# Performance work log

Hardware: AMD Instinct MI355X
Metric: run time of the kernel (lower is better)

Reference implementation:

```python
import jax, jax.numpy as jnp
import numpy as np

EMBED_DIM = 128
HEADS = 1
HEAD_DIM = EMBED_DIM // HEADS
TOPK = 3


def setup_inputs() -> dict:
    key = jax.random.key(0)
    k1, k2, k3, k4, k5 = jax.random.split(key, 5)
    N, T, C = 8, 2048, EMBED_DIM
    s = 1.0 / np.sqrt(C)
    return {
        "embeddings": jax.random.normal(k1, (N, T, C), dtype=jnp.float32),
        "ac": jax.random.normal(k2, (N,), dtype=jnp.float32),  # unused by forward (as in source)
        "Wq": jax.random.normal(k3, (C, C), dtype=jnp.float32) * s,
        "Wk": jax.random.normal(k4, (C, C), dtype=jnp.float32) * s,
        "Wo": jax.random.normal(k5, (C, C), dtype=jnp.float32) * s,
        "bo": jnp.zeros((C,), dtype=jnp.float32),
    }


def reference(embeddings, ac, Wq, Wk, Wo, bo):
    N, T, C = embeddings.shape
    H, D = HEADS, HEAD_DIM
    # values are the raw embeddings (no projection), per the source
    values = embeddings.reshape(N, T, H, D)
    keys = (embeddings @ Wk.T).reshape(N, T, H, D)
    queries = (embeddings @ Wq.T).reshape(N, T, H, D)
    # [N,H,T,T] dense scores, scaled by sqrt(embed_dim)
    scores = jnp.einsum('nqhd,nkhd->nhqk', queries, keys) / jnp.sqrt(jnp.float32(C))
    # top-3 masking: keep top-3 per row, -inf elsewhere, then softmax
    topv, topi = jax.lax.top_k(scores, TOPK)  # [N,H,T,3]
    ni = jnp.arange(N)[:, None, None, None]
    hi = jnp.arange(H)[None, :, None, None]
    qi = jnp.arange(T)[None, None, :, None]
    masked = jnp.full(scores.shape, -jnp.inf, scores.dtype).at[ni, hi, qi, topi].set(topv)
    attention = jax.nn.softmax(masked, axis=-1)  # [N,H,T,T]
    out = jnp.einsum('nhql,nlhd->nqhd', attention, values).reshape(N, T, H * D)
    out = out @ Wo.T + bo
    return out, attention
```

## Files before the change

### kernel.cpp

```cpp
#include <hip/hip_runtime.h>
#include <stdint.h>

#define TS 2048
#define CD 128
#define NB 8
#define NROWS (NB*TS)
#define RPB 8
#define SCALE 0.08838834764831845f

#define JSPLIT 8
#define QT 64
#define KT 32
#define KRANGE (TS/JSPLIT)
#define NKT (KRANGE/KT)
#define CSTR 97

typedef _Float16 f16x8 __attribute__((ext_vector_type(8)));
typedef float    f32x4 __attribute__((ext_vector_type(4)));

__device__ __forceinline__ void gload_lds16(const void* g, void* l) {
    __builtin_amdgcn_global_load_lds(
        (const __attribute__((address_space(1))) void*)g,
        (__attribute__((address_space(3))) void*)l, 16, 0, 0);
}

__global__ __launch_bounds__(128) void proj_qk(
    const float* __restrict__ E, const float* __restrict__ Wq,
    const float* __restrict__ Wk, _Float16* __restrict__ Qc, _Float16* __restrict__ Kc)
{
    const int r0 = blockIdx.x * RPB, t = threadIdx.x;
    __shared__ float e[RPB][CD];
    {
        const float4* src = (const float4*)(E + (size_t)r0*CD);
        float4* dst = (float4*)&e[0][0];
        dst[t] = src[t];
        dst[t + 128] = src[t + 128];
    }
    __syncthreads();
    const float* wq = Wq + (size_t)t*CD;
    const float* wk = Wk + (size_t)t*CD;
    float aq[RPB], ak[RPB];
    #pragma unroll
    for (int i = 0; i < RPB; i++) { aq[i] = 0.f; ak[i] = 0.f; }
    #pragma unroll
    for (int c = 0; c < CD; c += 4) {
        float4 a = *(const float4*)(wq + c);
        float4 b = *(const float4*)(wk + c);
        #pragma unroll
        for (int i = 0; i < RPB; i++) {
            float e0 = e[i][c+0], e1 = e[i][c+1], e2 = e[i][c+2], e3 = e[i][c+3];
            aq[i] += a.x*e0 + a.y*e1 + a.z*e2 + a.w*e3;
            ak[i] += b.x*e0 + b.y*e1 + b.z*e2 + b.w*e3;
        }
    }
    #pragma unroll
    for (int i = 0; i < RPB; i++) {
        float q = aq[i], k = ak[i];
        _Float16 qh = (_Float16)q, kh = (_Float16)k;
        _Float16 ql = (_Float16)(q - (float)qh);
        _Float16 kl = (_Float16)(k - (float)kh);
        const size_t rb = (size_t)(r0+i)*256;
        Qc[rb + t] = qh; Qc[rb + 128 + t] = ql;
        Kc[rb + t] = kh; Kc[rb + 128 + t] = kl;
    }
}

#define UPD(v, jg, s) do { \
    if ((v) > tv2[s]) { \
        if ((v) > tv0[s]) { tv2[s]=tv1[s]; ti2[s]=ti1[s]; tv1[s]=tv0[s]; ti1[s]=ti0[s]; tv0[s]=(v); ti0[s]=(jg); } \
        else if ((v) > tv1[s]) { tv2[s]=tv1[s]; ti2[s]=ti1[s]; tv1[s]=(v); ti1[s]=(jg); } \
        else { tv2[s]=(v); ti2[s]=(jg); } \
    } \
} while (0)

__global__ __launch_bounds__(256, 4) void scores_top3(
    const _Float16* __restrict__ Qc, const _Float16* __restrict__ Kc,
    float* __restrict__ SPL)
{
    const int bid = blockIdx.x;
    const int swz = (bid & 7) * 256 + (bid >> 3);
    const int n  = swz >> 8;
    const int sp = (swz >> 5) & 7;
    const int qt = swz & 31;
    const int q0 = qt * QT;
    const int j0 = sp * KRANGE;
    const int tid = threadIdx.x;
    const int w = tid >> 6, l = tid & 63;
    const int m = l & 15, hi = l >> 4;

    __shared__ __align__(16) char lds[32768];

    f16x8 qa[2][4];
    {
        const char* qb = (const char*)Qc + (size_t)(n*TS + q0 + w*16)*512;
        #pragma unroll
        for (int h = 0; h < 2; h++)
            #pragma unroll
            for (int c4 = 0; c4 < 4; c4++)
                qa[h][c4] = *(const f16x8*)(qb + m*512 + h*256 + c4*64 + hi*16);
    }

    const char* kcb = (const char*)Kc + (size_t)(n*TS + j0)*512;
    const char* ps[4];
    {
        const int ksub = l >> 5, coff = (l & 31) * 16;
        #pragma unroll
        for (int i = 0; i < 4; i++) {
            const int key = w*8 + i*2 + ksub;
            ps[i] = kcb + key*512 + (coff ^ ((i*2 + ksub) << 4));
        }
    }
    char* ldsw = lds + w*4096;

    float tv0[4], tv1[4], tv2[4];
    int   ti0[4], ti1[4], ti2[4];
    #pragma unroll
    for (int s = 0; s < 4; s++) {
        tv0[s]=tv1[s]=tv2[s] = -3e38f;
        ti0[s]=ti1[s]=ti2[s] = 0x7fffffff;
    }

    #pragma unroll
    for (int i = 0; i < 4; i++)
        gload_lds16(ps[i], ldsw + i*1024);

    const int swzl = (l & 7) << 4;
    const int lo16 = hi << 4;

    int cur = 0;
    #pragma unroll 1
    for (int kt = 0; kt < NKT; kt++) {
        __syncthreads();
        if (kt + 1 < NKT) {
            char* d_ = ldsw + ((cur^1) << 14);
            #pragma unroll
            for (int i = 0; i < 4; i++)
                gload_lds16(ps[i] + (size_t)(kt+1)*16384, d_ + i*1024);
        }
        const char* kb = lds + (cur << 14);

        f32x4 acc[2];
        acc[0] = (f32x4){0.f,0.f,0.f,0.f};
        acc[1] = (f32x4){0.f,0.f,0.f,0.f};

        __builtin_amdgcn_s_setprio(1);
        #pragma unroll
        for (int ct = 0; ct < 2; ct++) {
            const char* bb = kb + (size_t)(ct*16 + m)*512;
            f16x8 kh[4];
            #pragma unroll
            for (int c4 = 0; c4 < 4; c4++)
                kh[c4] = *(const f16x8*)(bb + ((c4*64 + lo16) ^ swzl));
            #pragma unroll
            for (int c4 = 0; c4 < 4; c4++)
                acc[ct] = __builtin_amdgcn_mfma_f32_16x16x32_f16(qa[0][c4], kh[c4], acc[ct], 0,0,0);
            #pragma unroll
            for (int c4 = 0; c4 < 4; c4++)
                acc[ct] = __builtin_amdgcn_mfma_f32_16x16x32_f16(qa[1][c4], kh[c4], acc[ct], 0,0,0);
            #pragma unroll
            for (int c4 = 0; c4 < 4; c4++) {
                f16x8 kl = *(const f16x8*)(bb + ((256 + c4*64 + lo16) ^ swzl));
                acc[ct] = __builtin_amdgcn_mfma_f32_16x16x32_f16(qa[0][c4], kl, acc[ct], 0,0,0);
            }
        }
        __builtin_amdgcn_s_setprio(0);

        const int jb = j0 + kt*KT;
        #pragma unroll
        for (int rg = 0; rg < 4; rg++) {
            float a0 = acc[0][rg], a1 = acc[1][rg];
            float mx = fmaxf(a0, a1);
            if (mx > tv2[rg]) {
                UPD(a0, jb + m, rg);
                UPD(a1, jb + 16 + m, rg);
            }
        }
        cur ^= 1;
    }

    __syncthreads();
    float* cand = (float*)lds;
    #pragma unroll
    for (int rg = 0; rg < 4; rg++) {
        const int row = w*16 + hi*4 + rg;
        float* cc = cand + row*CSTR + m*6;
        cc[0] = tv0[rg]; cc[1] = __int_as_float(ti0[rg]);
        cc[2] = tv1[rg]; cc[3] = __int_as_float(ti1[rg]);
        cc[4] = tv2[rg]; cc[5] = __int_as_float(ti2[rg]);
    }
    __syncthreads();
    if (tid < QT) {
        float b0v = -3e38f, b1v = -3e38f, b2v = -3e38f;
        int   b0i = 0x7fffffff, b1i = 0x7fffffff, b2i = 0x7fffffff;
        const float* mm = cand + (size_t)tid*CSTR;
        for (int t2 = 0; t2 < 16; t2++) {
            #pragma unroll
            for (int k = 0; k < 3; k++) {
                float v = mm[t2*6 + 2*k];
                int  id = __float_as_int(mm[t2*6 + 2*k + 1]);
                bool g2 = (v > b2v) || (v == b2v && id < b2i);
                if (g2) {
                    bool g0 = (v > b0v) || (v == b0v && id < b0i);
                    bool g1 = (v > b1v) || (v == b1v && id < b1i);
                    if (g0)      { b2v=b1v;b2i=b1i; b1v=b0v;b1i=b0i; b0v=v;b0i=id; }
                    else if (g1) { b2v=b1v;b2i=b1i; b1v=v;  b1i=id; }
                    else         { b2v=v;  b2i=id; }
                }
            }
        }
        const int row = n*TS + q0 + tid;
        float* dst = SPL + ((size_t)row*JSPLIT + sp)*8;
        dst[0] = b0v; dst[1] = __int_as_float(b0i);
        dst[2] = b1v; dst[3] = __int_as_float(b1i);
        dst[4] = b2v; dst[5] = __int_as_float(b2i);
    }
}

__global__ __launch_bounds__(256) void merge_splits(
    const float* __restrict__ SPL, float* __restrict__ TOP)
{
    const int row = blockIdx.x*256 + threadIdx.x;
    const float* s = SPL + (size_t)row*JSPLIT*8;
    float b0v = -3e38f, b1v = -3e38f, b2v = -3e38f;
    int   b0i = 0x7fffffff, b1i = 0x7fffffff, b2i = 0x7fffffff;
    #pragma unroll
    for (int sp = 0; sp < JSPLIT; sp++) {
        #pragma unroll
        for (int k = 0; k < 3; k++) {
            float v = s[sp*8 + 2*k];
            int  id = __float_as_int(s[sp*8 + 2*k + 1]);
            bool g2 = (v > b2v) || (v == b2v && id < b2i);
            if (g2) {
                bool g0 = (v > b0v) || (v == b0v && id < b0i);
                bool g1 = (v > b1v) || (v == b1v && id < b1i);
                if (g0)      { b2v=b1v;b2i=b1i; b1v=b0v;b1i=b0i; b0v=v;b0i=id; }
                else if (g1) { b2v=b1v;b2i=b1i; b1v=v;  b1i=id; }
                else         { b2v=v;  b2i=id; }
            }
        }
    }
    float e1 = __expf((b1v - b0v)*SCALE);
    float e2 = __expf((b2v - b0v)*SCALE);
    float rz = 1.0f / (1.0f + e1 + e2);
    float* dst = TOP + (size_t)row*8;
    dst[0] = rz; dst[1] = e1*rz; dst[2] = e2*rz;
    int* di = (int*)dst;
    di[4] = b0i; di[5] = b1i; di[6] = b2i;
}

__global__ __launch_bounds__(256) void attn_write(
    const float* __restrict__ TOP, float* __restrict__ A)
{
    const int r = blockIdx.x, t = threadIdx.x;
    const float* s = TOP + (size_t)r*8;
    const int* si = (const int*)s;
    float p0 = s[0], p1 = s[1], p2 = s[2];
    int i0 = si[4], i1 = si[5], i2 = si[6];
    const int col0 = t*8;
    float vals[8];
    #pragma unroll
    for (int u = 0; u < 8; u++) {
        int col = col0 + u;
        float v = 0.f;
        if (col == i0) v = p0;
        if (col == i1) v = p1;
        if (col == i2) v = p2;
        vals[u] = v;
    }
    float4* dst = (float4*)(A + (size_t)r*TS + col0);
    dst[0] = make_float4(vals[0], vals[1], vals[2], vals[3]);
    dst[1] = make_float4(vals[4], vals[5], vals[6], vals[7]);
}

__global__ __launch_bounds__(128) void out_proj(
    const float* __restrict__ E, const float* __restrict__ Wo,
    const float* __restrict__ bo, const float* __restrict__ TOP,
    float* __restrict__ OUT)
{
    const int r0 = blockIdx.x * RPB, t = threadIdx.x;
    const int n = r0 >> 11;
    __shared__ float o[RPB][CD];
    #pragma unroll
    for (int i = 0; i < RPB; i++) {
        const float* s = TOP + (size_t)(r0+i)*8;
        const int* si = (const int*)s;
        const float* e0 = E + ((size_t)n*TS + si[4])*CD;
        const float* e1 = E + ((size_t)n*TS + si[5])*CD;
        const float* e2 = E + ((size_t)n*TS + si[6])*CD;
        o[i][t] = s[0]*e0[t] + s[1]*e1[t] + s[2]*e2[t];
    }
    __syncthreads();
    const float* wr = Wo + (size_t)t*CD;
    float acc[RPB];
    float bias = bo[t];
    #pragma unroll
    for (int i = 0; i < RPB; i++) acc[i] = bias;
    #pragma unroll
    for (int c = 0; c < CD; c += 4) {
        float4 a = *(const float4*)(wr + c);
        #pragma unroll
        for (int i = 0; i < RPB; i++)
            acc[i] += a.x*o[i][c+0] + a.y*o[i][c+1] + a.z*o[i][c+2] + a.w*o[i][c+3];
    }
    #pragma unroll
    for (int i = 0; i < RPB; i++)
        OUT[(size_t)(r0+i)*CD + t] = acc[i];
}

extern "C" void kernel_launch(void* const* d_in, const int* in_sizes, int n_in,
                              void* d_out, int out_size, void* d_ws, size_t ws_size,
                              hipStream_t stream)
{
    const float* E  = (const float*)d_in[0];
    const float* Wq = (const float*)d_in[2];
    const float* Wk = (const float*)d_in[3];
    const float* Wo = (const float*)d_in[4];
    const float* bo = (const float*)d_in[5];

    _Float16* Qc = (_Float16*)d_ws;
    _Float16* Kc = Qc + (size_t)NROWS*256;
    float* TOP   = (float*)(Kc + (size_t)NROWS*256);

    float* OUT = (float*)d_out;
    float* A   = OUT + (size_t)NROWS*CD;
    float* SPL = A;

    proj_qk     <<<NROWS/RPB, 128, 0, stream>>>(E, Wq, Wk, Qc, Kc);
    scores_top3 <<<NB*(TS/QT)*JSPLIT, 256, 0, stream>>>(Qc, Kc, SPL);
    merge_splits<<<NROWS/256, 256, 0, stream>>>(SPL, TOP);
    attn_write  <<<NROWS,     256, 0, stream>>>(TOP, A);
    out_proj    <<<NROWS/RPB, 128, 0, stream>>>(E, Wo, bo, TOP, OUT);
}
```

Before: 284.5 us.

## Double query tile per block and fuse split merge into attention write

The scores kernel now gives each wave 32 query rows instead of 16, so every K fragment read from LDS feeds twice as many MFMAs, and the K tile is shared across 128 queries per block. That halves K global/LDS traffic per query but raises register pressure, and occupancy is lowered to 3 blocks per CU. When the workspace is large enough, split candidates go to workspace instead of the attention buffer, and the merge plus dense attention write become one kernel. This removes one launch and the TOP round trip at the cost of every thread redundantly merging its row's splits.

```diff
diff --git a/kernel.cpp b/kernel.cpp
--- a/kernel.cpp
+++ b/kernel.cpp
@@ -9,11 +9,12 @@
 #define SCALE 0.08838834764831845f
 
 #define JSPLIT 8
-#define QT 64
+#define QT 128
 #define KT 32
 #define KRANGE (TS/JSPLIT)
 #define NKT (KRANGE/KT)
 #define CSTR 97
+#define LDS_BYTES 49664
 
 typedef _Float16 f16x8 __attribute__((ext_vector_type(8)));
 typedef float    f32x4 __attribute__((ext_vector_type(4)));
@@ -73,56 +74,58 @@
     } \
 } while (0)
 
-__global__ __launch_bounds__(256, 4) void scores_top3(
+__global__ __launch_bounds__(256, 3) void scores_top3(
     const _Float16* __restrict__ Qc, const _Float16* __restrict__ Kc,
     float* __restrict__ SPL)
 {
     const int bid = blockIdx.x;
-    const int swz = (bid & 7) * 256 + (bid >> 3);
-    const int n  = swz >> 8;
-    const int sp = (swz >> 5) & 7;
-    const int qt = swz & 31;
+    const int swz = (bid & 7) * 128 + (bid >> 3);
+    const int n  = swz >> 7;
+    const int sp = (swz >> 4) & 7;
+    const int qt = swz & 15;
     const int q0 = qt * QT;
     const int j0 = sp * KRANGE;
     const int tid = threadIdx.x;
     const int w = tid >> 6, l = tid & 63;
     const int m = l & 15, hi = l >> 4;
 
-    __shared__ __align__(16) char lds[32768];
-
-    f16x8 qa[2][4];
+    __shared__ __align__(16) char lds[LDS_BYTES];
+
+    f16x8 qa[2][2][4];
     {
-        const char* qb = (const char*)Qc + (size_t)(n*TS + q0 + w*16)*512;
-        #pragma unroll
-        for (int h = 0; h < 2; h++)
-            #pragma unroll
-            for (int c4 = 0; c4 < 4; c4++)
-                qa[h][c4] = *(const f16x8*)(qb + m*512 + h*256 + c4*64 + hi*16);
+        const char* qb = (const char*)Qc + (size_t)(n*TS + q0 + w*32)*512;
+        #pragma unroll
+        for (int rt = 0; rt < 2; rt++)
+            #pragma unroll
+            for (int h = 0; h < 2; h++)
+                #pragma unroll
+                for (int c4 = 0; c4 < 4; c4++)
+                    qa[rt][h][c4] = *(const f16x8*)(qb + (rt*16 + m)*512 + h*256 + c4*64 + hi*16);
     }
 
     const char* kcb = (const char*)Kc + (size_t)(n*TS + j0)*512;
-    const char* ps[4];
+    int off[4];
     {
         const int ksub = l >> 5, coff = (l & 31) * 16;
         #pragma unroll
         for (int i = 0; i < 4; i++) {
             const int key = w*8 + i*2 + ksub;
-            ps[i] = kcb + key*512 + (coff ^ ((i*2 + ksub) << 4));
+            off[i] = key*512 + (coff ^ ((i*2 + ksub) << 4));
         }
     }
     char* ldsw = lds + w*4096;
 
-    float tv0[4], tv1[4], tv2[4];
-    int   ti0[4], ti1[4], ti2[4];
-    #pragma unroll
-    for (int s = 0; s < 4; s++) {
+    float tv0[8], tv1[8], tv2[8];
+    int   ti0[8], ti1[8], ti2[8];
+    #pragma unroll
+    for (int s = 0; s < 8; s++) {
         tv0[s]=tv1[s]=tv2[s] = -3e38f;
         ti0[s]=ti1[s]=ti2[s] = 0x7fffffff;
     }
 
     #pragma unroll
     for (int i = 0; i < 4; i++)
-        gload_lds16(ps[i], ldsw + i*1024);
+        gload_lds16(kcb + off[i], ldsw + i*1024);
 
     const int swzl = (l & 7) << 4;
     const int lo16 = hi << 4;
@@ -133,61 +136,67 @@
         __syncthreads();
         if (kt + 1 < NKT) {
             char* d_ = ldsw + ((cur^1) << 14);
+            const char* s_ = kcb + (size_t)(kt+1)*16384;
             #pragma unroll
             for (int i = 0; i < 4; i++)
-                gload_lds16(ps[i] + (size_t)(kt+1)*16384, d_ + i*1024);
+                gload_lds16(s_ + off[i], d_ + i*1024);
         }
         const char* kb = lds + (cur << 14);
 
-        f32x4 acc[2];
-        acc[0] = (f32x4){0.f,0.f,0.f,0.f};
-        acc[1] = (f32x4){0.f,0.f,0.f,0.f};
+        f32x4 acc[2][2];
+        #pragma unroll
+        for (int rt = 0; rt < 2; rt++)
+            #pragma unroll
+            for (int ct = 0; ct < 2; ct++)
+                acc[rt][ct] = (f32x4){0.f,0.f,0.f,0.f};
 
         __builtin_amdgcn_s_setprio(1);
         #pragma unroll
         for (int ct = 0; ct < 2; ct++) {
             const char* bb = kb + (size_t)(ct*16 + m)*512;
-            f16x8 kh[4];
-            #pragma unroll
-            for (int c4 = 0; c4 < 4; c4++)
-                kh[c4] = *(const f16x8*)(bb + ((c4*64 + lo16) ^ swzl));
-            #pragma unroll
-            for (int c4 = 0; c4 < 4; c4++)
-                acc[ct] = __builtin_amdgcn_mfma_f32_16x16x32_f16(qa[0][c4], kh[c4], acc[ct], 0,0,0);
-            #pragma unroll
-            for (int c4 = 0; c4 < 4; c4++)
-                acc[ct] = __builtin_amdgcn_mfma_f32_16x16x32_f16(qa[1][c4], kh[c4], acc[ct], 0,0,0);
             #pragma unroll
             for (int c4 = 0; c4 < 4; c4++) {
+                f16x8 kh = *(const f16x8*)(bb + ((c4*64 + lo16) ^ swzl));
                 f16x8 kl = *(const f16x8*)(bb + ((256 + c4*64 + lo16) ^ swzl));
-                acc[ct] = __builtin_amdgcn_mfma_f32_16x16x32_f16(qa[0][c4], kl, acc[ct], 0,0,0);
+                acc[0][ct] = __builtin_amdgcn_mfma_f32_16x16x32_f16(qa[0][0][c4], kh, acc[0][ct], 0,0,0);
+                acc[1][ct] = __builtin_amdgcn_mfma_f32_16x16x32_f16(qa[1][0][c4], kh, acc[1][ct], 0,0,0);
+                acc[0][ct] = __builtin_amdgcn_mfma_f32_16x16x32_f16(qa[0][1][c4], kh, acc[0][ct], 0,0,0);
+                acc[1][ct] = __builtin_amdgcn_mfma_f32_16x16x32_f16(qa[1][1][c4], kh, acc[1][ct], 0,0,0);
+                acc[0][ct] = __builtin_amdgcn_mfma_f32_16x16x32_f16(qa[0][0][c4], kl, acc[0][ct], 0,0,0);
+                acc[1][ct] = __builtin_amdgcn_mfma_f32_16x16x32_f16(qa[1][0][c4], kl, acc[1][ct], 0,0,0);
             }
         }
         __builtin_amdgcn_s_setprio(0);
 
         const int jb = j0 + kt*KT;
         #pragma unroll
-        for (int rg = 0; rg < 4; rg++) {
-            float a0 = acc[0][rg], a1 = acc[1][rg];
-            float mx = fmaxf(a0, a1);
-            if (mx > tv2[rg]) {
-                UPD(a0, jb + m, rg);
-                UPD(a1, jb + 16 + m, rg);
+        for (int rt = 0; rt < 2; rt++)
+            #pragma unroll
+            for (int rg = 0; rg < 4; rg++) {
+                const int s = rt*4 + rg;
+                float a0 = acc[rt][0][rg], a1 = acc[rt][1][rg];
+                float mx = fmaxf(a0, a1);
+                if (mx > tv2[s]) {
+                    UPD(a0, jb + m, s);
+                    UPD(a1, jb + 16 + m, s);
+                }
             }
-        }
         cur ^= 1;
     }
 
     __syncthreads();
     float* cand = (float*)lds;
     #pragma unroll
-    for (int rg = 0; rg < 4; rg++) {
-        const int row = w*16 + hi*4 + rg;
-        float* cc = cand + row*CSTR + m*6;
-        cc[0] = tv0[rg]; cc[1] = __int_as_float(ti0[rg]);
-        cc[2] = tv1[rg]; cc[3] = __int_as_float(ti1[rg]);
-        cc[4] = tv2[rg]; cc[5] = __int_as_float(ti2[rg]);
-    }
+    for (int rt = 0; rt < 2; rt++)
+        #pragma unroll
+        for (int rg = 0; rg < 4; rg++) {
+            const int s = rt*4 + rg;
+            const int row = w*32 + rt*16 + hi*4 + rg;
+            float* cc = cand + row*CSTR + m*6;
+            cc[0] = tv0[s]; cc[1] = __int_as_float(ti0[s]);
+            cc[2] = tv1[s]; cc[3] = __int_as_float(ti1[s]);
+            cc[4] = tv2[s]; cc[5] = __int_as_float(ti2[s]);
+        }
     __syncthreads();
     if (tid < QT) {
         float b0v = -3e38f, b1v = -3e38f, b2v = -3e38f;
@@ -216,11 +225,11 @@
     }
 }
 
-__global__ __launch_bounds__(256) void merge_splits(
-    const float* __restrict__ SPL, float* __restrict__ TOP)
-{
-    const int row = blockIdx.x*256 + threadIdx.x;
-    const float* s = SPL + (size_t)row*JSPLIT*8;
+__global__ __launch_bounds__(256) void finalize_write(
+    const float* __restrict__ SPL, float* __restrict__ TOP, float* __restrict__ A)
+{
+    const int r = blockIdx.x, t = threadIdx.x;
+    const float* s = SPL + (size_t)r*JSPLIT*8;
     float b0v = -3e38f, b1v = -3e38f, b2v = -3e38f;
     int   b0i = 0x7fffffff, b1i = 0x7fffffff, b2i = 0x7fffffff;
     #pragma unroll
@@ -242,6 +251,57 @@
     float e1 = __expf((b1v - b0v)*SCALE);
     float e2 = __expf((b2v - b0v)*SCALE);
     float rz = 1.0f / (1.0f + e1 + e2);
+    float p0 = rz, p1 = e1*rz, p2 = e2*rz;
+    if (t == 0) {
+        float* dst = TOP + (size_t)r*8;
+        dst[0] = p0; dst[1] = p1; dst[2] = p2;
+        int* di = (int*)dst;
+        di[4] = b0i; di[5] = b1i; di[6] = b2i;
+    }
+    const int col0 = t*8;
+    float vals[8];
+    #pragma unroll
+    for (int u = 0; u < 8; u++) {
+        int col = col0 + u;
+        float v = 0.f;
+        if (col == b0i) v = p0;
+        if (col == b1i) v = p1;
+        if (col == b2i) v = p2;
+        vals[u] = v;
+    }
+    f32x4* dst = (f32x4*)(A + (size_t)r*TS + col0);
+    f32x4 v0 = {vals[0], vals[1], vals[2], vals[3]};
+    f32x4 v1 = {vals[4], vals[5], vals[6], vals[7]};
+    __builtin_nontemporal_store(v0, dst);
+    __builtin_nontemporal_store(v1, dst + 1);
+}
+
+__global__ __launch_bounds__(256) void merge_splits(
+    const float* __restrict__ SPL, float* __restrict__ TOP)
+{
+    const int row = blockIdx.x*256 + threadIdx.x;
+    const float* s = SPL + (size_t)row*JSPLIT*8;
+    float b0v = -3e38f, b1v = -3e38f, b2v = -3e38f;
+    int   b0i = 0x7fffffff, b1i = 0x7fffffff, b2i = 0x7fffffff;
+    #pragma unroll
+    for (int sp = 0; sp < JSPLIT; sp++) {
+        #pragma unroll
+        for (int k = 0; k < 3; k++) {
+            float v = s[sp*8 + 2*k];
+            int  id = __float_as_int(s[sp*8 + 2*k + 1]);
+            bool g2 = (v > b2v) || (v == b2v && id < b2i);
+            if (g2) {
+                bool g0 = (v > b0v) || (v == b0v && id < b0i);
+                bool g1 = (v > b1v) || (v == b1v && id < b1i);
+                if (g0)      { b2v=b1v;b2i=b1i; b1v=b0v;b1i=b0i; b0v=v;b0i=id; }
+                else if (g1) { b2v=b1v;b2i=b1i; b1v=v;  b1i=id; }
+                else         { b2v=v;  b2i=id; }
+            }
+        }
+    }
+    float e1 = __expf((b1v - b0v)*SCALE);
+    float e2 = __expf((b2v - b0v)*SCALE);
+    float rz = 1.0f / (1.0f + e1 + e2);
     float* dst = TOP + (size_t)row*8;
     dst[0] = rz; dst[1] = e1*rz; dst[2] = e2*rz;
     int* di = (int*)dst;
@@ -323,11 +383,18 @@
 
     float* OUT = (float*)d_out;
     float* A   = OUT + (size_t)NROWS*CD;
-    float* SPL = A;
+
+    const size_t need = (size_t)NROWS*512*2 + (size_t)NROWS*32 + (size_t)NROWS*256;
+    const bool fused = ws_size >= need;
+    float* SPL = fused ? (TOP + (size_t)NROWS*8) : A;
 
     proj_qk     <<<NROWS/RPB, 128, 0, stream>>>(E, Wq, Wk, Qc, Kc);
     scores_top3 <<<NB*(TS/QT)*JSPLIT, 256, 0, stream>>>(Qc, Kc, SPL);
-    merge_splits<<<NROWS/256, 256, 0, stream>>>(SPL, TOP);
-    attn_write  <<<NROWS,     256, 0, stream>>>(TOP, A);
+    if (fused) {
+        finalize_write<<<NROWS, 256, 0, stream>>>(SPL, TOP, A);
+    } else {
+        merge_splits<<<NROWS/256, 256, 0, stream>>>(SPL, TOP);
+        attn_write  <<<NROWS,     256, 0, stream>>>(TOP, A);
+    }
     out_proj    <<<NROWS/RPB, 128, 0, stream>>>(E, Wo, bo, TOP, OUT);
 }
```

New measurement: 356.1 us. 1.25x slower.

## Compute Q/K projection with split-fp16 MFMA instead of scalar FP32 FMAs

Applied to the files above, without the earlier changes.

Replaces the scalar FP32 Q/K projection kernel with an MFMA kernel. Embeddings and weights are split into hi/lo fp16 pairs, and three MFMA products (hi*hi, hi*lo, lo*hi) approximate the fp32 result. A new small kernel converts Wq/Wk to hi/lo fp16 form each call. The aim is to cut projection time using matrix cores. In exchange it adds an extra launch and a small loss of precision from the dropped lo*lo term.

```diff
diff --git a/kernel.cpp b/kernel.cpp
--- a/kernel.cpp
+++ b/kernel.cpp
@@ -16,6 +16,7 @@
 #define CSTR 97
 
 typedef _Float16 f16x8 __attribute__((ext_vector_type(8)));
+typedef _Float16 f16x4 __attribute__((ext_vector_type(4)));
 typedef float    f32x4 __attribute__((ext_vector_type(4)));
 
 __device__ __forceinline__ void gload_lds16(const void* g, void* l) {
@@ -24,44 +25,75 @@
         (__attribute__((address_space(3))) void*)l, 16, 0, 0);
 }
 
-__global__ __launch_bounds__(128) void proj_qk(
-    const float* __restrict__ E, const float* __restrict__ Wq,
-    const float* __restrict__ Wk, _Float16* __restrict__ Qc, _Float16* __restrict__ Kc)
-{
-    const int r0 = blockIdx.x * RPB, t = threadIdx.x;
-    __shared__ float e[RPB][CD];
+__global__ __launch_bounds__(128) void wconv(
+    const float* __restrict__ Wq, const float* __restrict__ Wk,
+    _Float16* __restrict__ Wqc, _Float16* __restrict__ Wkc)
+{
+    const int o = blockIdx.x & 127, mat = blockIdx.x >> 7, t = threadIdx.x;
+    const float* src = (mat ? Wk : Wq) + (size_t)o*CD;
+    _Float16* dst = (mat ? Wkc : Wqc) + (size_t)o*256;
+    float v = src[t];
+    _Float16 h = (_Float16)v;
+    dst[t] = h;
+    dst[128 + t] = (_Float16)(v - (float)h);
+}
+
+__global__ __launch_bounds__(256) void proj_mfma(
+    const float* __restrict__ E, const _Float16* __restrict__ Wqc,
+    const _Float16* __restrict__ Wkc,
+    _Float16* __restrict__ Qc, _Float16* __restrict__ Kc)
+{
+    const int tid = threadIdx.x, w = tid >> 6, l = tid & 63;
+    const int m = l & 15, hi = l >> 4;
+    const int r = blockIdx.x*64 + w*16 + m;
+
+    f16x8 eb[2][4];
     {
-        const float4* src = (const float4*)(E + (size_t)r0*CD);
-        float4* dst = (float4*)&e[0][0];
-        dst[t] = src[t];
-        dst[t + 128] = src[t + 128];
-    }
-    __syncthreads();
-    const float* wq = Wq + (size_t)t*CD;
-    const float* wk = Wk + (size_t)t*CD;
-    float aq[RPB], ak[RPB];
-    #pragma unroll
-    for (int i = 0; i < RPB; i++) { aq[i] = 0.f; ak[i] = 0.f; }
-    #pragma unroll
-    for (int c = 0; c < CD; c += 4) {
-        float4 a = *(const float4*)(wq + c);
-        float4 b = *(const float4*)(wk + c);
-        #pragma unroll
-        for (int i = 0; i < RPB; i++) {
-            float e0 = e[i][c+0], e1 = e[i][c+1], e2 = e[i][c+2], e3 = e[i][c+3];
-            aq[i] += a.x*e0 + a.y*e1 + a.z*e2 + a.w*e3;
-            ak[i] += b.x*e0 + b.y*e1 + b.z*e2 + b.w*e3;
-        }
-    }
-    #pragma unroll
-    for (int i = 0; i < RPB; i++) {
-        float q = aq[i], k = ak[i];
-        _Float16 qh = (_Float16)q, kh = (_Float16)k;
-        _Float16 ql = (_Float16)(q - (float)qh);
-        _Float16 kl = (_Float16)(k - (float)kh);
-        const size_t rb = (size_t)(r0+i)*256;
-        Qc[rb + t] = qh; Qc[rb + 128 + t] = ql;
-        Kc[rb + t] = kh; Kc[rb + 128 + t] = kl;
+        const float* er = E + (size_t)r*CD;
+        #pragma unroll
+        for (int c4 = 0; c4 < 4; c4++) {
+            float4 x = *(const float4*)(er + c4*32 + hi*8);
+            float4 y = *(const float4*)(er + c4*32 + hi*8 + 4);
+            float v[8] = {x.x,x.y,x.z,x.w,y.x,y.y,y.z,y.w};
+            f16x8 hh, ll;
+            #pragma unroll
+            for (int j = 0; j < 8; j++) {
+                _Float16 h2 = (_Float16)v[j];
+                hh[j] = h2;
+                ll[j] = (_Float16)(v[j] - (float)h2);
+            }
+            eb[0][c4] = hh; eb[1][c4] = ll;
+        }
+    }
+
+    #pragma unroll
+    for (int mat = 0; mat < 2; mat++) {
+        const char* wc = (const char*)(mat ? Wkc : Wqc);
+        _Float16* dst = mat ? Kc : Qc;
+        #pragma unroll 2
+        for (int ct = 0; ct < 8; ct++) {
+            const char* wb = wc + (size_t)(ct*16 + m)*512 + hi*16;
+            f32x4 acc = (f32x4){0.f,0.f,0.f,0.f};
+            #pragma unroll
+            for (int c4 = 0; c4 < 4; c4++) {
+                f16x8 wh = *(const f16x8*)(wb + c4*64);
+                f16x8 wl = *(const f16x8*)(wb + 256 + c4*64);
+                acc = __builtin_amdgcn_mfma_f32_16x16x32_f16(wh, eb[0][c4], acc, 0,0,0);
+                acc = __builtin_amdgcn_mfma_f32_16x16x32_f16(wh, eb[1][c4], acc, 0,0,0);
+                acc = __builtin_amdgcn_mfma_f32_16x16x32_f16(wl, eb[0][c4], acc, 0,0,0);
+            }
+            f16x4 hv, lv;
+            #pragma unroll
+            for (int g = 0; g < 4; g++) {
+                float q = acc[g];
+                _Float16 h2 = (_Float16)q;
+                hv[g] = h2;
+                lv[g] = (_Float16)(q - (float)h2);
+            }
+            char* db = (char*)dst + (size_t)r*512 + ct*32 + hi*8;
+            *(f16x4*)db = hv;
+            *(f16x4*)(db + 256) = lv;
+        }
     }
 }
 
@@ -320,14 +352,17 @@
     _Float16* Qc = (_Float16*)d_ws;
     _Float16* Kc = Qc + (size_t)NROWS*256;
     float* TOP   = (float*)(Kc + (size_t)NROWS*256);
+    _Float16* Wqc = (_Float16*)(TOP + (size_t)NROWS*8);
+    _Float16* Wkc = Wqc + 128*256;
 
     float* OUT = (float*)d_out;
     float* A   = OUT + (size_t)NROWS*CD;
     float* SPL = A;
 
-    proj_qk     <<<NROWS/RPB, 128, 0, stream>>>(E, Wq, Wk, Qc, Kc);
+    wconv       <<<256,        128, 0, stream>>>(Wq, Wk, Wqc, Wkc);
+    proj_mfma   <<<NROWS/64,   256, 0, stream>>>(E, Wqc, Wkc, Qc, Kc);
     scores_top3 <<<NB*(TS/QT)*JSPLIT, 256, 0, stream>>>(Qc, Kc, SPL);
-    merge_splits<<<NROWS/256, 256, 0, stream>>>(SPL, TOP);
-    attn_write  <<<NROWS,     256, 0, stream>>>(TOP, A);
-    out_proj    <<<NROWS/RPB, 128, 0, stream>>>(E, Wo, bo, TOP, OUT);
-}
+    merge_splits<<<NROWS/256,  256, 0, stream>>>(SPL, TOP);
+    attn_write  <<<NROWS,      256, 0, stream>>>(TOP, A);
+    out_proj    <<<NROWS/RPB,  128, 0, stream>>>(E, Wo, bo, TOP, OUT);
+}
```

Result: faster. 271.1 us (-4.7%).
